# Kernel optimization log

Measured on AMD Instinct MI355X. Metric: run time of the kernel, lower is better.

Reference implementation:

```python
import jax, jax.numpy as jnp
import numpy as np

N_NODES = 50000
N_EDGES = 1600000
F_IN = 384
NR_SIGMOID = 1  # hidden_sizes[-1]


def setup_inputs() -> dict:
    key = jax.random.key(0)
    ks = jax.random.split(key, 8)
    x = jax.random.normal(ks[0], (N_NODES, F_IN), jnp.float32)
    edge_index = jax.random.randint(ks[1], (2, N_EDGES), 0, N_NODES, jnp.int32)
    def lin(k, fin, fout):
        return jax.random.normal(k, (fin, fout), jnp.float32) / np.sqrt(fin).astype(np.float32)
    W1 = lin(ks[2], F_IN, 64)
    W2 = lin(ks[3], 64, 32)
    W3 = lin(ks[4], 32, 1 + F_IN)  # reconstruction=True: last width = 1 + input_size
    return {
        "x": x, "edge_index": edge_index,
        "W1": W1, "b1": jnp.zeros((64,), jnp.float32),
        "W2": W2, "b2": jnp.zeros((32,), jnp.float32),
        "W3": W3, "b3": jnp.zeros((1 + F_IN,), jnp.float32),
    }


def reference(x, edge_index, W1, b1, W2, b2, W3, b3):
    N = x.shape[0]
    self_loop = jnp.arange(N, dtype=edge_index.dtype)
    src = jnp.concatenate([edge_index[0], self_loop])  # [E+N]
    dst = jnp.concatenate([edge_index[1], self_loop])
    # symmetric GCN normalization (with self-loops), as in PyG GCNConv
    deg = jax.ops.segment_sum(jnp.ones(dst.shape[0], x.dtype), dst, num_segments=N)
    dinv = jnp.where(deg > 0, jax.lax.rsqrt(deg), 0.0)
    norm = (dinv[src] * dinv[dst])[:, None]  # [E+N, 1]

    def gcn_conv(h, W, b):
        m = h @ W                         # transform first (fewer message bytes)
        agg = jax.ops.segment_sum(m[src] * norm, dst, num_segments=N)
        return agg + b

    h = jax.nn.relu(gcn_conv(x, W1, b1))
    h = jax.nn.relu(gcn_conv(h, W2, b2))
    h = gcn_conv(h, W3, b3)
    # sigmoid on the first nr_sigmoid_layers columns only
    return jnp.concatenate([jax.nn.sigmoid(h[:, :NR_SIGMOID]), h[:, NR_SIGMOID:]], axis=1)
```

## Files before the change

kernel.cpp:

```cpp
#include <hip/hip_runtime.h>

#define F_IN  384
#define EPB   4096
#define NBINS 256
#define BCAP  12288
#define SDS   208

typedef __attribute__((ext_vector_type(8))) short short8v;
typedef __attribute__((ext_vector_type(4))) float f32x4;

__device__ __forceinline__ unsigned short f2bf(float f) {
    unsigned u = __float_as_uint(f);
    return (unsigned short)((u + 0x7FFFu + ((u >> 16) & 1u)) >> 16);
}
__device__ __forceinline__ float bflo(unsigned u) { return __uint_as_float(u << 16); }
__device__ __forceinline__ float bfhi(unsigned u) { return __uint_as_float(u & 0xFFFF0000u); }


__launch_bounds__(256)
__global__ void k_p1(const int* __restrict__ ei, int E, int NBK,
                     unsigned* __restrict__ packed, unsigned short* __restrict__ segdesc) {
    __shared__ unsigned sin[EPB];
    __shared__ unsigned sout[EPB];
    __shared__ int hist[257], cur[256], excl[257];
    const int t = threadIdx.x;
    const int e0 = blockIdx.x * EPB;
    const int cnt = min(EPB, E - e0);

    if (t < 256) { hist[t] = 0; cur[t] = 0; }
    if (t == 0) hist[256] = 0;
    __syncthreads();

    for (int i = t; i < cnt; i += 256) {
        int s = ei[e0 + i];
        int d = ei[E + e0 + i];
        sin[i] = ((unsigned)d << 16) | (unsigned)s;
        atomicAdd(&hist[d >> 8], 1);
    }
    __syncthreads();

    if (t < 64) {
        int carry = 0;
        for (int c = 0; c * 64 < NBK; ++c) {
            int idx = c * 64 + t;
            int v = (idx < NBK) ? hist[idx] : 0;
            int x = v;
#pragma unroll
            for (int d = 1; d < 64; d <<= 1) { int y = __shfl_up(x, d, 64); if (t >= d) x += y; }
            if (idx < NBK) excl[idx] = carry + x - v;
            carry += __shfl(x, 63, 64);
        }
        if (t == 0) excl[NBK] = carry;
    }
    __syncthreads();

    for (int i = t; i < cnt; i += 256) {
        unsigned v = sin[i];
        int b = v >> 24;
        int pos = excl[b] + atomicAdd(&cur[b], 1);
        sout[pos] = v;
    }
    __syncthreads();

    for (int i = t; i < cnt; i += 256) packed[(size_t)e0 + i] = sout[i];
    for (int i = t; i <= NBK; i += 256) segdesc[(size_t)blockIdx.x * SDS + i] = (unsigned short)excl[i];
}


__launch_bounds__(256)
__global__ void k_p2(const unsigned* __restrict__ packed, const unsigned short* __restrict__ segdesc,
                     int NB1, unsigned short* __restrict__ eidx,
                     int* __restrict__ rpB, int* __restrict__ rpE,
                     float* __restrict__ dinv, int N) {
    __shared__ unsigned ev[BCAP];
    __shared__ unsigned short se[BCAP];
    __shared__ int lenS[512], offS[513];
    __shared__ int hist[NBINS], cur[NBINS], excl[NBINS + 1];
    const int t = threadIdx.x;
    const int b = blockIdx.x;

    if (t < NBINS) { hist[t] = 0; cur[t] = 0; }
    for (int blk = t; blk < NB1; blk += 256) {
        int s0 = segdesc[(size_t)blk * SDS + b];
        int s1 = segdesc[(size_t)blk * SDS + b + 1];
        lenS[blk] = s1 - s0;
    }
    __syncthreads();

    if (t < 64) {
        int carry = 0;
        for (int c = 0; c * 64 < NB1; ++c) {
            int idx = c * 64 + t;
            int v = (idx < NB1) ? lenS[idx] : 0;
            int x = v;
#pragma unroll
            for (int d = 1; d < 64; d <<= 1) { int y = __shfl_up(x, d, 64); if (t >= d) x += y; }
            if (idx < NB1) offS[idx] = carry + x - v;
            carry += __shfl(x, 63, 64);
        }
        if (t == 0) offS[NB1 < 512 ? NB1 : 512] = carry;
    }
    __syncthreads();
    const int total = min(offS[NB1 < 512 ? NB1 : 512], BCAP);

    for (int blk = t; blk < NB1; blk += 256) {
        int s0 = segdesc[(size_t)blk * SDS + b];
        int l = lenS[blk], o = offS[blk];
        if (o + l > BCAP) l = max(0, BCAP - o);
        const unsigned* sp = packed + (size_t)blk * EPB + s0;
        for (int j = 0; j < l; ++j) ev[o + j] = sp[j];
    }
    __syncthreads();

    for (int i = t; i < total; i += 256) atomicAdd(&hist[(ev[i] >> 16) & 0xFF], 1);
    __syncthreads();

    if (t < 64) {
        int carry = 0;
#pragma unroll
        for (int c = 0; c < 4; ++c) {
            int idx = c * 64 + t;
            int v = hist[idx];
            int x = v;
#pragma unroll
            for (int d = 1; d < 64; d <<= 1) { int y = __shfl_up(x, d, 64); if (t >= d) x += y; }
            excl[idx] = carry + x - v;
            carry += __shfl(x, 63, 64);
        }
        if (t == 0) excl[NBINS] = carry;
    }
    __syncthreads();

    if (t < NBINS) {
        int d = b * NBINS + t;
        if (d < N) {
            int c = hist[t];
            int base = b * BCAP + excl[t];
            rpB[d] = base;
            rpE[d] = base + c;
            dinv[d] = rsqrtf((float)(c + 1));
        }
    }
    for (int i = t; i < total; i += 256) {
        unsigned v = ev[i];
        int l = (v >> 16) & 0xFF;
        int p = excl[l] + atomicAdd(&cur[l], 1);
        se[p] = (unsigned short)(v & 0xFFFF);
    }
    __syncthreads();
    for (int i = t; i < total; i += 256) eidx[(size_t)b * BCAP + i] = se[i];
}


__launch_bounds__(256)
__global__ void k_gemm1(const float* __restrict__ x, const float* __restrict__ W1,
                        const float* __restrict__ dinv,
                        unsigned short* __restrict__ m1p, int N) {
    __shared__ __align__(16) unsigned short xb[64][136];
    __shared__ __align__(16) unsigned short wb[64][136];
    const int t    = threadIdx.x;
    const int lane = t & 63;
    const int wv   = t >> 6;
    const int lr   = lane & 15;
    const int kg   = lane >> 4;
    const int row0 = blockIdx.x * 64;

    f32x4 acc[4];
#pragma unroll
    for (int rb = 0; rb < 4; rb++) acc[rb] = (f32x4){0.f, 0.f, 0.f, 0.f};

    for (int k0 = 0; k0 < F_IN; k0 += 128) {
#pragma unroll
        for (int i = 0; i < 4; i++) {
            int g  = t + i * 256;
            int r  = g >> 4;
            int gk = (g & 15) << 3;
            int row = row0 + r;
            short8v p = (short8v){0, 0, 0, 0, 0, 0, 0, 0};
            if (row < N) {
                const float* sp = &x[(size_t)row * F_IN + k0 + gk];
                float4 f0 = *reinterpret_cast<const float4*>(sp);
                float4 f1 = *reinterpret_cast<const float4*>(sp + 4);
                p[0] = (short)f2bf(f0.x); p[1] = (short)f2bf(f0.y);
                p[2] = (short)f2bf(f0.z); p[3] = (short)f2bf(f0.w);
                p[4] = (short)f2bf(f1.x); p[5] = (short)f2bf(f1.y);
                p[6] = (short)f2bf(f1.z); p[7] = (short)f2bf(f1.w);
            }
            *reinterpret_cast<short8v*>(&xb[r][gk]) = p;
        }
#pragma unroll
        for (int i = 0; i < 4; i++) {
            int g  = t + i * 256;
            int k  = g >> 3;
            int c0 = (g & 7) << 3;
            const float* sp = &W1[(size_t)(k0 + k) * 64 + c0];
            float4 f0 = *reinterpret_cast<const float4*>(sp);
            float4 f1 = *reinterpret_cast<const float4*>(sp + 4);
            wb[c0 + 0][k] = f2bf(f0.x); wb[c0 + 1][k] = f2bf(f0.y);
            wb[c0 + 2][k] = f2bf(f0.z); wb[c0 + 3][k] = f2bf(f0.w);
            wb[c0 + 4][k] = f2bf(f1.x); wb[c0 + 5][k] = f2bf(f1.y);
            wb[c0 + 6][k] = f2bf(f1.z); wb[c0 + 7][k] = f2bf(f1.w);
        }
        __syncthreads();

#pragma unroll
        for (int kk = 0; kk < 128; kk += 32) {
            short8v bfrag = *reinterpret_cast<const short8v*>(&wb[(wv << 4) + lr][kk + (kg << 3)]);
#pragma unroll
            for (int rb = 0; rb < 4; rb++) {
                short8v afrag = *reinterpret_cast<const short8v*>(&xb[(rb << 4) + lr][kk + (kg << 3)]);
                acc[rb] = __builtin_amdgcn_mfma_f32_16x16x32_bf16(afrag, bfrag, acc[rb], 0, 0, 0);
            }
        }
        __syncthreads();
    }

    const int col = (wv << 4) + lr;
#pragma unroll
    for (int rb = 0; rb < 4; rb++) {
#pragma unroll
        for (int i = 0; i < 4; i++) {
            int row = row0 + (rb << 4) + (kg << 2) + i;
            if (row < N) m1p[(size_t)row * 64 + col] = f2bf(acc[rb][i] * dinv[row]);
        }
    }
}


__launch_bounds__(256)
__global__ void k_gather64h(const int* __restrict__ rpB, const int* __restrict__ rpE,
                            const unsigned short* __restrict__ eidx,
                            const unsigned* __restrict__ msg,
                            float* __restrict__ acc, int N) {
    int w = blockIdx.x * 8 + (threadIdx.x >> 5);
    if (w >= N) return;
    int f = threadIdx.x & 31;
    int i = rpB[w], e = rpE[w];
    unsigned u = msg[(size_t)w * 32 + f];
    float l0 = bflo(u), h0 = bfhi(u);
    float l1 = 0.f, h1 = 0.f, l2 = 0.f, h2 = 0.f, l3 = 0.f, h3 = 0.f;
    for (; i + 4 <= e; i += 4) {
        unsigned u0 = msg[(size_t)eidx[i]     * 32 + f];
        unsigned u1 = msg[(size_t)eidx[i + 1] * 32 + f];
        unsigned u2 = msg[(size_t)eidx[i + 2] * 32 + f];
        unsigned u3 = msg[(size_t)eidx[i + 3] * 32 + f];
        l0 += bflo(u0); h0 += bfhi(u0);
        l1 += bflo(u1); h1 += bfhi(u1);
        l2 += bflo(u2); h2 += bfhi(u2);
        l3 += bflo(u3); h3 += bfhi(u3);
    }
    for (; i < e; i++) {
        unsigned u0 = msg[(size_t)eidx[i] * 32 + f];
        l0 += bflo(u0); h0 += bfhi(u0);
    }
    *reinterpret_cast<float2*>(&acc[(size_t)w * 64 + (f << 1)]) =
        make_float2((l0 + l1) + (l2 + l3), (h0 + h1) + (h2 + h3));
}


__launch_bounds__(256)
__global__ void k_gather32h(const int* __restrict__ rpB, const int* __restrict__ rpE,
                            const unsigned short* __restrict__ eidx,
                            const unsigned* __restrict__ msg,
                            void* __restrict__ outp, int N,
                            const float* __restrict__ bias, const float* __restrict__ dinv,
                            const float* __restrict__ W3, const float* __restrict__ b3,
                            float* __restrict__ out) {
    int w = blockIdx.x * 16 + (threadIdx.x >> 4);
    if (w >= N) return;
    int f = threadIdx.x & 15;
    int i = rpB[w], e = rpE[w];
    unsigned u = msg[(size_t)w * 16 + f];
    float l0 = bflo(u), h0 = bfhi(u);
    float l1 = 0.f, h1 = 0.f, l2 = 0.f, h2 = 0.f, l3 = 0.f, h3 = 0.f;
    for (; i + 4 <= e; i += 4) {
        unsigned u0 = msg[(size_t)eidx[i]     * 16 + f];
        unsigned u1 = msg[(size_t)eidx[i + 1] * 16 + f];
        unsigned u2 = msg[(size_t)eidx[i + 2] * 16 + f];
        unsigned u3 = msg[(size_t)eidx[i + 3] * 16 + f];
        l0 += bflo(u0); h0 += bfhi(u0);
        l1 += bflo(u1); h1 += bfhi(u1);
        l2 += bflo(u2); h2 += bfhi(u2);
        l3 += bflo(u3); h3 += bfhi(u3);
    }
    for (; i < e; i++) {
        unsigned u0 = msg[(size_t)eidx[i] * 16 + f];
        l0 += bflo(u0); h0 += bfhi(u0);
    }
    float rl = (l0 + l1) + (l2 + l3);
    float rh = (h0 + h1) + (h2 + h3);
    float s = dinv[w];
    if (bias) {
        rl = fmaxf(rl * s + bias[(f << 1)], 0.f) * s;
        rh = fmaxf(rh * s + bias[(f << 1) + 1], 0.f) * s;
        ((unsigned*)outp)[(size_t)w * 16 + f] = (unsigned)f2bf(rl) | ((unsigned)f2bf(rh) << 16);
    } else {
        float gl = rl * s, gh = rh * s;
        ((unsigned*)outp)[(size_t)w * 16 + f] = (unsigned)f2bf(gl) | ((unsigned)f2bf(gh) << 16);
        float p = gl * W3[(size_t)(2 * f) * 385 + 384] + gh * W3[(size_t)(2 * f + 1) * 385 + 384];
#pragma unroll
        for (int m = 8; m >= 1; m >>= 1) p += __shfl_xor(p, m, 64);
        if (f == 0) out[(size_t)w * 385 + 384] = p + b3[384];
    }
}


__launch_bounds__(256)
__global__ void k_layer2(const float* __restrict__ acc1, const float* __restrict__ W2,
                         const float* __restrict__ b1, const float* __restrict__ dinv,
                         unsigned short* __restrict__ m2p, int N) {
    __shared__ float h1t[64][64];
    __shared__ float w2t[64][32];
    const int t = threadIdx.x;
    const int row0 = blockIdx.x * 64;
#pragma unroll
    for (int i = 0; i < 16; i++) {
        int lin = i * 256 + t;
        int r = lin >> 6, c = lin & 63;
        int row = row0 + r;
        float v = 0.f;
        if (row < N) v = fmaxf(acc1[(size_t)row * 64 + c] * dinv[row] + b1[c], 0.f);
        h1t[r][c] = v;
    }
#pragma unroll
    for (int i = 0; i < 8; i++) {
        int lin = i * 256 + t;
        w2t[lin >> 5][lin & 31] = W2[lin];
    }
    __syncthreads();
    const int tx = t & 31, ty = t >> 5;
#pragma unroll
    for (int rr = 0; rr < 8; rr++) {
        int r = rr * 8 + ty;
        float a = 0.f;
#pragma unroll
        for (int k = 0; k < 64; k++) a += h1t[r][k] * w2t[k][tx];
        int row = row0 + r;
        if (row < N) m2p[(size_t)row * 32 + tx] = f2bf(a * dinv[row]);
    }
}


__launch_bounds__(256)
__global__ void k_out(const unsigned* __restrict__ gbf, const float* __restrict__ W3,
                      const float* __restrict__ b3, float* __restrict__ out, int N) {
    const int t    = threadIdx.x;
    const int lane = t & 63;
    const int wv   = t >> 6;
    const int lr   = lane & 15;
    const int kg   = lane >> 4;
    const int row0 = blockIdx.x * 64;
    const int col  = blockIdx.y * 64 + (wv << 4) + lr;

    short8v bfrag;
#pragma unroll
    for (int j = 0; j < 8; j++)
        bfrag[j] = (short)f2bf(W3[(size_t)((kg << 3) + j) * 385 + col]);
    const float bias = b3[col];

#pragma unroll
    for (int rb = 0; rb < 4; rb++) {
        int arow = row0 + (rb << 4) + lr;
        short8v afrag = (short8v){0, 0, 0, 0, 0, 0, 0, 0};
        if (arow < N)
            afrag = *reinterpret_cast<const short8v*>(&gbf[(size_t)arow * 16 + (kg << 2)]);
        f32x4 acc = (f32x4){0.f, 0.f, 0.f, 0.f};
        acc = __builtin_amdgcn_mfma_f32_16x16x32_bf16(afrag, bfrag, acc, 0, 0, 0);
#pragma unroll
        for (int i = 0; i < 4; i++) {
            int row = row0 + (rb << 4) + (kg << 2) + i;
            if (row < N) {
                float v = acc[i] + bias;
                if (col == 0) v = 1.0f / (1.0f + expf(-v));
                out[(size_t)row * 385 + col] = v;
            }
        }
    }
}

extern "C" void kernel_launch(void* const* d_in, const int* in_sizes, int n_in,
                              void* d_out, int out_size, void* d_ws, size_t ws_size,
                              hipStream_t stream) {
    const float* x  = (const float*)d_in[0];
    const int*   ei = (const int*)d_in[1];
    const float* W1 = (const float*)d_in[2];
    const float* b1 = (const float*)d_in[3];
    const float* W2 = (const float*)d_in[4];
    const float* b2 = (const float*)d_in[5];
    const float* W3 = (const float*)d_in[6];
    const float* b3 = (const float*)d_in[7];
    float* out = (float*)d_out;

    const int N = in_sizes[0] / F_IN;
    const int E = in_sizes[1] / 2;
    const int NB1 = (E + EPB - 1) / EPB;
    const int NBK = (N + NBINS - 1) / NBINS;

    float* ws   = (float*)d_ws;
    float* dinv = ws;
    float* bufA = ws + N;
    float* bufB = bufA + (size_t)64 * N;
    int*   rpB  = (int*)(bufB + (size_t)64 * N);
    int*   rpE  = rpB + N;
    unsigned short* eidx    = (unsigned short*)(rpE + N);
    unsigned short* segdesc = eidx + (size_t)NBK * BCAP;

    unsigned* packed = (unsigned*)bufA;
    unsigned short* m1p = (unsigned short*)bufA;
    float* acc1 = bufB;
    unsigned short* m2p = (unsigned short*)bufA;
    unsigned short* h2p = (unsigned short*)bufB;
    unsigned* gbf = (unsigned*)(bufA + (size_t)32 * N);

    k_p1<<<NB1, 256, 0, stream>>>(ei, E, NBK, packed, segdesc);
    k_p2<<<NBK, 256, 0, stream>>>(packed, segdesc, NB1, eidx, rpB, rpE, dinv, N);

    k_gemm1    <<<(N + 63) / 64, 256, 0, stream>>>(x, W1, dinv, m1p, N);
    k_gather64h<<<(N + 7) / 8, 256, 0, stream>>>(rpB, rpE, eidx, (const unsigned*)m1p, acc1, N);

    k_layer2   <<<(N + 63) / 64, 256, 0, stream>>>(acc1, W2, b1, dinv, m2p, N);
    k_gather32h<<<(N + 15) / 16, 256, 0, stream>>>(rpB, rpE, eidx, (const unsigned*)m2p,
                                                   (void*)h2p, N, b2, dinv, nullptr, nullptr, nullptr);

    k_gather32h<<<(N + 15) / 16, 256, 0, stream>>>(rpB, rpE, eidx, (const unsigned*)h2p,
                                                   (void*)gbf, N, nullptr, dinv, W3, b3, out);

    dim3 gout((N + 63) / 64, 6);
    k_out<<<gout, 256, 0, stream>>>(gbf, W3, b3, out, N);
}
```

Measured before the change: 176.2 us.

## Fuse layer-1 epilogue into gather, bf16 hidden, MFMA layer-2 GEMM, 8-way unroll

The layer-1 gather now applies dinv, bias and ReLU itself and writes the hidden state as packed bf16 instead of fp32 partial sums. That halves the intermediate traffic and drops the elementwise pass from layer 2. Layer 2 is rewritten from an LDS fp32 GEMM into bf16 MFMA 16x16x32 instructions that read the bf16 hidden directly. Both gather kernels also gain an 8-way unrolled edge loop for more memory-level parallelism. The cost is extra rounding of the hidden activations to bf16 and higher register use in the gathers.

Result: faster. 154.2 us (-12.5%).

```diff
diff --git a/kernel.cpp b/kernel.cpp
--- a/kernel.cpp
+++ b/kernel.cpp
@@ -228,10 +228,11 @@
 
 
 __launch_bounds__(256)
-__global__ void k_gather64h(const int* __restrict__ rpB, const int* __restrict__ rpE,
-                            const unsigned short* __restrict__ eidx,
-                            const unsigned* __restrict__ msg,
-                            float* __restrict__ acc, int N) {
+__global__ void k_g64l1(const int* __restrict__ rpB, const int* __restrict__ rpE,
+                        const unsigned short* __restrict__ eidx,
+                        const unsigned* __restrict__ msg,
+                        const float* __restrict__ b1, const float* __restrict__ dinv,
+                        unsigned* __restrict__ m1h, int N) {
     int w = blockIdx.x * 8 + (threadIdx.x >> 5);
     if (w >= N) return;
     int f = threadIdx.x & 31;
@@ -239,22 +240,39 @@
     unsigned u = msg[(size_t)w * 32 + f];
     float l0 = bflo(u), h0 = bfhi(u);
     float l1 = 0.f, h1 = 0.f, l2 = 0.f, h2 = 0.f, l3 = 0.f, h3 = 0.f;
+    float l4 = 0.f, h4 = 0.f, l5 = 0.f, h5 = 0.f, l6 = 0.f, h6 = 0.f, l7 = 0.f, h7 = 0.f;
+    for (; i + 8 <= e; i += 8) {
+        unsigned u0 = msg[(size_t)eidx[i]     * 32 + f];
+        unsigned u1 = msg[(size_t)eidx[i + 1] * 32 + f];
+        unsigned u2 = msg[(size_t)eidx[i + 2] * 32 + f];
+        unsigned u3 = msg[(size_t)eidx[i + 3] * 32 + f];
+        unsigned u4 = msg[(size_t)eidx[i + 4] * 32 + f];
+        unsigned u5 = msg[(size_t)eidx[i + 5] * 32 + f];
+        unsigned u6 = msg[(size_t)eidx[i + 6] * 32 + f];
+        unsigned u7 = msg[(size_t)eidx[i + 7] * 32 + f];
+        l0 += bflo(u0); h0 += bfhi(u0);  l1 += bflo(u1); h1 += bfhi(u1);
+        l2 += bflo(u2); h2 += bfhi(u2);  l3 += bflo(u3); h3 += bfhi(u3);
+        l4 += bflo(u4); h4 += bfhi(u4);  l5 += bflo(u5); h5 += bfhi(u5);
+        l6 += bflo(u6); h6 += bfhi(u6);  l7 += bflo(u7); h7 += bfhi(u7);
+    }
     for (; i + 4 <= e; i += 4) {
         unsigned u0 = msg[(size_t)eidx[i]     * 32 + f];
         unsigned u1 = msg[(size_t)eidx[i + 1] * 32 + f];
         unsigned u2 = msg[(size_t)eidx[i + 2] * 32 + f];
         unsigned u3 = msg[(size_t)eidx[i + 3] * 32 + f];
-        l0 += bflo(u0); h0 += bfhi(u0);
-        l1 += bflo(u1); h1 += bfhi(u1);
-        l2 += bflo(u2); h2 += bfhi(u2);
-        l3 += bflo(u3); h3 += bfhi(u3);
+        l0 += bflo(u0); h0 += bfhi(u0);  l1 += bflo(u1); h1 += bfhi(u1);
+        l2 += bflo(u2); h2 += bfhi(u2);  l3 += bflo(u3); h3 += bfhi(u3);
     }
     for (; i < e; i++) {
         unsigned u0 = msg[(size_t)eidx[i] * 32 + f];
         l0 += bflo(u0); h0 += bfhi(u0);
     }
-    *reinterpret_cast<float2*>(&acc[(size_t)w * 64 + (f << 1)]) =
-        make_float2((l0 + l1) + (l2 + l3), (h0 + h1) + (h2 + h3));
+    float suml = ((l0 + l1) + (l2 + l3)) + ((l4 + l5) + (l6 + l7));
+    float sumh = ((h0 + h1) + (h2 + h3)) + ((h4 + h5) + (h6 + h7));
+    float s = dinv[w];
+    float hl = fmaxf(suml * s + b1[(f << 1)], 0.f);
+    float hh = fmaxf(sumh * s + b1[(f << 1) + 1], 0.f);
+    m1h[(size_t)w * 32 + f] = (unsigned)f2bf(hl) | ((unsigned)f2bf(hh) << 16);
 }
 
 
@@ -273,22 +291,35 @@
     unsigned u = msg[(size_t)w * 16 + f];
     float l0 = bflo(u), h0 = bfhi(u);
     float l1 = 0.f, h1 = 0.f, l2 = 0.f, h2 = 0.f, l3 = 0.f, h3 = 0.f;
+    float l4 = 0.f, h4 = 0.f, l5 = 0.f, h5 = 0.f, l6 = 0.f, h6 = 0.f, l7 = 0.f, h7 = 0.f;
+    for (; i + 8 <= e; i += 8) {
+        unsigned u0 = msg[(size_t)eidx[i]     * 16 + f];
+        unsigned u1 = msg[(size_t)eidx[i + 1] * 16 + f];
+        unsigned u2 = msg[(size_t)eidx[i + 2] * 16 + f];
+        unsigned u3 = msg[(size_t)eidx[i + 3] * 16 + f];
+        unsigned u4 = msg[(size_t)eidx[i + 4] * 16 + f];
+        unsigned u5 = msg[(size_t)eidx[i + 5] * 16 + f];
+        unsigned u6 = msg[(size_t)eidx[i + 6] * 16 + f];
+        unsigned u7 = msg[(size_t)eidx[i + 7] * 16 + f];
+        l0 += bflo(u0); h0 += bfhi(u0);  l1 += bflo(u1); h1 += bfhi(u1);
+        l2 += bflo(u2); h2 += bfhi(u2);  l3 += bflo(u3); h3 += bfhi(u3);
+        l4 += bflo(u4); h4 += bfhi(u4);  l5 += bflo(u5); h5 += bfhi(u5);
+        l6 += bflo(u6); h6 += bfhi(u6);  l7 += bflo(u7); h7 += bfhi(u7);
+    }
     for (; i + 4 <= e; i += 4) {
         unsigned u0 = msg[(size_t)eidx[i]     * 16 + f];
         unsigned u1 = msg[(size_t)eidx[i + 1] * 16 + f];
         unsigned u2 = msg[(size_t)eidx[i + 2] * 16 + f];
         unsigned u3 = msg[(size_t)eidx[i + 3] * 16 + f];
-        l0 += bflo(u0); h0 += bfhi(u0);
-        l1 += bflo(u1); h1 += bfhi(u1);
-        l2 += bflo(u2); h2 += bfhi(u2);
-        l3 += bflo(u3); h3 += bfhi(u3);
+        l0 += bflo(u0); h0 += bfhi(u0);  l1 += bflo(u1); h1 += bfhi(u1);
+        l2 += bflo(u2); h2 += bfhi(u2);  l3 += bflo(u3); h3 += bfhi(u3);
     }
     for (; i < e; i++) {
         unsigned u0 = msg[(size_t)eidx[i] * 16 + f];
         l0 += bflo(u0); h0 += bfhi(u0);
     }
-    float rl = (l0 + l1) + (l2 + l3);
-    float rh = (h0 + h1) + (h2 + h3);
+    float rl = ((l0 + l1) + (l2 + l3)) + ((l4 + l5) + (l6 + l7));
+    float rh = ((h0 + h1) + (h2 + h3)) + ((h4 + h5) + (h6 + h7));
     float s = dinv[w];
     if (bias) {
         rl = fmaxf(rl * s + bias[(f << 1)], 0.f) * s;
@@ -306,37 +337,49 @@
 
 
 __launch_bounds__(256)
-__global__ void k_layer2(const float* __restrict__ acc1, const float* __restrict__ W2,
-                         const float* __restrict__ b1, const float* __restrict__ dinv,
+__global__ void k_layer2(const unsigned* __restrict__ m1h, const float* __restrict__ W2,
+                         const float* __restrict__ dinv,
                          unsigned short* __restrict__ m2p, int N) {
-    __shared__ float h1t[64][64];
-    __shared__ float w2t[64][32];
-    const int t = threadIdx.x;
-    const int row0 = blockIdx.x * 64;
-#pragma unroll
-    for (int i = 0; i < 16; i++) {
-        int lin = i * 256 + t;
-        int r = lin >> 6, c = lin & 63;
-        int row = row0 + r;
-        float v = 0.f;
-        if (row < N) v = fmaxf(acc1[(size_t)row * 64 + c] * dinv[row] + b1[c], 0.f);
-        h1t[r][c] = v;
-    }
-#pragma unroll
-    for (int i = 0; i < 8; i++) {
-        int lin = i * 256 + t;
-        w2t[lin >> 5][lin & 31] = W2[lin];
-    }
-    __syncthreads();
-    const int tx = t & 31, ty = t >> 5;
-#pragma unroll
-    for (int rr = 0; rr < 8; rr++) {
-        int r = rr * 8 + ty;
-        float a = 0.f;
-#pragma unroll
-        for (int k = 0; k < 64; k++) a += h1t[r][k] * w2t[k][tx];
-        int row = row0 + r;
-        if (row < N) m2p[(size_t)row * 32 + tx] = f2bf(a * dinv[row]);
+    const int t    = threadIdx.x;
+    const int lane = t & 63;
+    const int wv   = t >> 6;
+    const int lr   = lane & 15;
+    const int kg   = lane >> 4;
+    const int row0 = blockIdx.x * 64 + (wv << 4);
+
+    short8v b00, b01, b10, b11;
+#pragma unroll
+    for (int j = 0; j < 8; j++) {
+        int k = (kg << 3) + j;
+        b00[j] = (short)f2bf(W2[(size_t)k * 32 + lr]);
+        b01[j] = (short)f2bf(W2[(size_t)k * 32 + 16 + lr]);
+        b10[j] = (short)f2bf(W2[(size_t)(32 + k) * 32 + lr]);
+        b11[j] = (short)f2bf(W2[(size_t)(32 + k) * 32 + 16 + lr]);
+    }
+
+    int arow = row0 + lr;
+    short8v a0 = (short8v){0, 0, 0, 0, 0, 0, 0, 0};
+    short8v a1 = (short8v){0, 0, 0, 0, 0, 0, 0, 0};
+    if (arow < N) {
+        a0 = *reinterpret_cast<const short8v*>(&m1h[(size_t)arow * 32 + (kg << 2)]);
+        a1 = *reinterpret_cast<const short8v*>(&m1h[(size_t)arow * 32 + 16 + (kg << 2)]);
+    }
+
+    f32x4 accA = (f32x4){0.f, 0.f, 0.f, 0.f};
+    f32x4 accB = (f32x4){0.f, 0.f, 0.f, 0.f};
+    accA = __builtin_amdgcn_mfma_f32_16x16x32_bf16(a0, b00, accA, 0, 0, 0);
+    accA = __builtin_amdgcn_mfma_f32_16x16x32_bf16(a1, b10, accA, 0, 0, 0);
+    accB = __builtin_amdgcn_mfma_f32_16x16x32_bf16(a0, b01, accB, 0, 0, 0);
+    accB = __builtin_amdgcn_mfma_f32_16x16x32_bf16(a1, b11, accB, 0, 0, 0);
+
+#pragma unroll
+    for (int i = 0; i < 4; i++) {
+        int row = row0 + (kg << 2) + i;
+        if (row < N) {
+            float s = dinv[row];
+            m2p[(size_t)row * 32 + lr]      = f2bf(accA[i] * s);
+            m2p[(size_t)row * 32 + 16 + lr] = f2bf(accB[i] * s);
+        }
     }
 }
 
@@ -407,7 +450,7 @@
 
     unsigned* packed = (unsigned*)bufA;
     unsigned short* m1p = (unsigned short*)bufA;
-    float* acc1 = bufB;
+    unsigned* m1h = (unsigned*)bufB;
     unsigned short* m2p = (unsigned short*)bufA;
     unsigned short* h2p = (unsigned short*)bufB;
     unsigned* gbf = (unsigned*)(bufA + (size_t)32 * N);
@@ -415,10 +458,10 @@
     k_p1<<<NB1, 256, 0, stream>>>(ei, E, NBK, packed, segdesc);
     k_p2<<<NBK, 256, 0, stream>>>(packed, segdesc, NB1, eidx, rpB, rpE, dinv, N);
 
-    k_gemm1    <<<(N + 63) / 64, 256, 0, stream>>>(x, W1, dinv, m1p, N);
-    k_gather64h<<<(N + 7) / 8, 256, 0, stream>>>(rpB, rpE, eidx, (const unsigned*)m1p, acc1, N);
-
-    k_layer2   <<<(N + 63) / 64, 256, 0, stream>>>(acc1, W2, b1, dinv, m2p, N);
+    k_gemm1   <<<(N + 63) / 64, 256, 0, stream>>>(x, W1, dinv, m1p, N);
+    k_g64l1   <<<(N + 7) / 8, 256, 0, stream>>>(rpB, rpE, eidx, (const unsigned*)m1p, b1, dinv, m1h, N);
+
+    k_layer2  <<<(N + 63) / 64, 256, 0, stream>>>(m1h, W2, dinv, m2p, N);
     k_gather32h<<<(N + 15) / 16, 256, 0, stream>>>(rpB, rpE, eidx, (const unsigned*)m2p,
                                                    (void*)h2p, N, b2, dinv, nullptr, nullptr, nullptr);
 
```
